# Kernel tuning notes

Hardware: AMD Instinct MI355X
Metric: run time of the kernel (lower is better)

Reference implementation:

```python
import jax, jax.numpy as jnp
import numpy as np

N_NODES = 50000
N_EDGES = 300000
IN_DIM = 2000
DF = 128
H1, H2, OUT_DIM, K = 256, 128, 32, 4


def gcn_conv(x, W, b, src, dst, ew):
    """PyG GCNConv with edge weights: add self-loops (weight 1), symmetric norm."""
    N = x.shape[0]
    loop = jnp.arange(N)
    src2 = jnp.concatenate([src, loop])
    dst2 = jnp.concatenate([dst, loop])
    ew2 = jnp.concatenate([ew, jnp.ones((N,), ew.dtype)])
    deg = jax.ops.segment_sum(ew2, dst2, num_segments=N)
    dinv = jnp.where(deg > 0, jax.lax.rsqrt(deg), 0.0)
    norm = dinv[src2] * ew2 * dinv[dst2]            # [E+N]
    h = x @ W                                       # [N, out]
    out = jax.ops.segment_sum(norm[:, None] * h[src2], dst2, num_segments=N)
    return out + b


def setup_inputs() -> dict:
    key = jax.random.key(0)
    ks = jax.random.split(key, 13)
    p = lambda k, shape, s=0.05: (jax.random.normal(k, shape, jnp.float32) * s)
    return {
        "X": jax.random.normal(ks[0], (N_NODES, IN_DIM), jnp.float32),
        "edge_index": jax.random.randint(ks[1], (2, N_EDGES), 0, N_NODES),
        "Wh": p(ks[2], (IN_DIM, DF)),
        "mlp_W1": p(ks[3], (K, 2 * DF, 2)),
        "mlp_b1": jnp.zeros((K, 2), jnp.float32),
        "mlp_W2": p(ks[4], (K, 2, 1)),
        "mlp_b2": jnp.zeros((K, 1), jnp.float32),
        "g1_W": p(ks[5], (DF, H1)),
        "g1_b": jnp.zeros((H1,), jnp.float32),
        "g2_W": p(ks[6], (H1, H2)),
        "g2_b": jnp.zeros((H2,), jnp.float32),
        "fc_W": p(ks[7], (H2, OUT_DIM)),
        "fc_b": jnp.zeros((OUT_DIM,), jnp.float32),
    }


def reference(X, edge_index, Wh, mlp_W1, mlp_b1, mlp_W2, mlp_b2,
              g1_W, g1_b, g2_W, g2_b, fc_W, fc_b):
    src, dst = edge_index[0], edge_index[1]
    h0 = X @ Wh                                          # [N, df]
    edge_h = jnp.concatenate([h0[src], h0[dst]], axis=1)  # [E, 2df]
    # all K per-edge MLPs at once: hidden dim is just 2
    hid = jax.nn.relu(jnp.einsum('ef,kfh->keh', edge_h, mlp_W1) + mlp_b1[:, None, :])
    Gk = jax.nn.sigmoid(jnp.einsum('keh,kho->keo', hid, mlp_W2) + mlp_b2[:, None, :])[..., 0]  # [K, E]

    def autoencoder(ew):
        z1 = jax.nn.relu(gcn_conv(h0, g1_W, g1_b, src, dst, ew))
        z2 = jax.nn.relu(gcn_conv(z1, g2_W, g2_b, src, dst, ew))
        return jnp.mean(z2, axis=0) @ fc_W + fc_b         # [out_dim]

    descriptors = jax.vmap(autoencoder)(Gk)               # [K, out_dim]
    return descriptors, Gk
```

## Files before the change

### kernel.cpp

```cpp
#include <hip/hip_runtime.h>

#define NN 50000
#define NE 300000
#define INDIM 2000
#define KPAD 2048

typedef float f32x4 __attribute__((ext_vector_type(4)));
typedef __bf16 bf16x8 __attribute__((ext_vector_type(8)));
typedef unsigned short u16x8 __attribute__((ext_vector_type(8)));

__device__ __forceinline__ unsigned short f2bf(float f) {
  union { float f; unsigned u; } v; v.f = f;
  unsigned r = v.u + 0x7FFFu + ((v.u >> 16) & 1u);
  return (unsigned short)(r >> 16);
}
__device__ __forceinline__ float bf2f(unsigned short h) {
  union { unsigned u; float f; } v; v.u = ((unsigned)h) << 16;
  return v.f;
}

__global__ __launch_bounds__(256) void prep_kernel(
    const float* __restrict__ Wh, const float* __restrict__ g1,
    const float* __restrict__ g2, const float* __restrict__ W1,
    unsigned short* __restrict__ WhT, unsigned short* __restrict__ g1T,
    unsigned short* __restrict__ g2T, float* __restrict__ Wc)
{
  int i = blockIdx.x * 256 + threadIdx.x;
  if (i < 128 * KPAD) {
    int n = i >> 11, k = i & (KPAD - 1);
    WhT[i] = (k < INDIM) ? f2bf(Wh[(size_t)k * 128 + n]) : (unsigned short)0;
    return;
  }
  i -= 128 * KPAD;
  if (i < 256 * 128) {
    int n = i >> 7, k = i & 127;
    g1T[i] = f2bf(g1[(size_t)k * 256 + n]);
    return;
  }
  i -= 256 * 128;
  if (i < 128 * 256) {
    int n = i >> 8, k = i & 255;
    g2T[i] = f2bf(g2[(size_t)k * 128 + n]);
    return;
  }
  i -= 128 * 256;
  if (i < 2048) {
    int f = i >> 4, o = i & 15;
    int k = (o & 7) >> 1, h = o & 1;
    int fr = (o < 8) ? f : (128 + f);
    Wc[i] = W1[(size_t)k * 512 + fr * 2 + h];
  }
}

template<int A_F32>
__global__ __launch_bounds__(256) void gemm_kernel(
    const void* __restrict__ Aptr, const unsigned short* __restrict__ BT,
    unsigned short* __restrict__ C, int M, int N, int Ka, int Kb, int nkb)
{
  __shared__ unsigned short Alds[128 * 64];
  __shared__ unsigned short Blds[128 * 64];
  const int tid = threadIdx.x, lane = tid & 63, wv = tid >> 6;
  const int mBase = blockIdx.x * 128, nBase = blockIdx.y * 128;
  const int wrow = (wv >> 1) * 64, wcol = (wv & 1) * 64;
  const int lr = lane >> 3, lk8 = (lane & 7) * 8;
  const int stIdx = (lr) * 64 + (((lane & 7) ^ lr) << 3);
  f32x4 acc[4][4] = {};

  for (int kb = 0; kb < nkb; ++kb) {
    int k0 = kb * 64;
    #pragma unroll
    for (int i = 0; i < 4; ++i) {
      int chunk = wv * 4 + i;
      int brow = chunk * 8 + lr;
      u16x8 v = *(const u16x8*)(BT + (size_t)(nBase + brow) * Kb + k0 + lk8);
      *(u16x8*)&Blds[chunk * 512 + stIdx] = v;
    }
    #pragma unroll
    for (int i = 0; i < 4; ++i) {
      int chunk = wv * 4 + i;
      int arow = chunk * 8 + lr;
      int rg = mBase + arow; if (rg > M - 1) rg = M - 1;
      u16x8 v;
      if (A_F32) {
        const float* Af = (const float*)Aptr;
        int kc = k0 + lk8; if (kc > Ka - 8) kc = Ka - 8;
        const float4* s = (const float4*)(Af + (size_t)rg * Ka + kc);
        float4 f0 = s[0], f1 = s[1];
        v[0]=f2bf(f0.x); v[1]=f2bf(f0.y); v[2]=f2bf(f0.z); v[3]=f2bf(f0.w);
        v[4]=f2bf(f1.x); v[5]=f2bf(f1.y); v[6]=f2bf(f1.z); v[7]=f2bf(f1.w);
      } else {
        const unsigned short* Ab = (const unsigned short*)Aptr;
        v = *(const u16x8*)(Ab + (size_t)rg * Ka + k0 + lk8);
      }
      *(u16x8*)&Alds[chunk * 512 + stIdx] = v;
    }
    __syncthreads();
    #pragma unroll
    for (int kk = 0; kk < 2; ++kk) {
      const int r16 = lane & 15;
      const int slot = kk * 4 + (lane >> 4);
      bf16x8 a[4], b[4];
      #pragma unroll
      for (int mf = 0; mf < 4; ++mf) {
        int row = wrow + mf * 16 + r16;
        a[mf] = __builtin_bit_cast(bf16x8,
            *(const u16x8*)&Alds[row * 64 + ((slot ^ (row & 7)) << 3)]);
      }
      #pragma unroll
      for (int nf = 0; nf < 4; ++nf) {
        int row = wcol + nf * 16 + r16;
        b[nf] = __builtin_bit_cast(bf16x8,
            *(const u16x8*)&Blds[row * 64 + ((slot ^ (row & 7)) << 3)]);
      }
      #pragma unroll
      for (int mf = 0; mf < 4; ++mf)
        #pragma unroll
        for (int nf = 0; nf < 4; ++nf)
          acc[mf][nf] = __builtin_amdgcn_mfma_f32_16x16x32_bf16(a[mf], b[nf], acc[mf][nf], 0, 0, 0);
    }
    __syncthreads();
  }

  const int r16 = lane & 15, r4 = (lane >> 4) * 4;
  #pragma unroll
  for (int mf = 0; mf < 4; ++mf) {
    #pragma unroll
    for (int j = 0; j < 4; ++j) {
      int row = mBase + wrow + mf * 16 + r4 + j;
      if (row < M) {
        #pragma unroll
        for (int nf = 0; nf < 4; ++nf) {
          int col = nBase + wcol + nf * 16 + r16;
          C[(size_t)row * N + col] = f2bf(acc[mf][nf][j]);
        }
      }
    }
  }
}

__global__ __launch_bounds__(256) void p_kernel(const unsigned short* __restrict__ h0,
    const float* __restrict__ Wc, float* __restrict__ P)
{
  __shared__ float wl[2048];
  for (int i = threadIdx.x; i < 2048; i += 256) wl[i] = Wc[i];
  __syncthreads();
  int n = blockIdx.x * 256 + threadIdx.x;
  if (n >= NN) return;
  const unsigned short* hr = h0 + (size_t)n * 128;
  float acc[16];
  #pragma unroll
  for (int o = 0; o < 16; ++o) acc[o] = 0.f;
  for (int f8 = 0; f8 < 128; f8 += 8) {
    u16x8 hv = *(const u16x8*)(hr + f8);
    #pragma unroll
    for (int j = 0; j < 8; ++j) {
      float v = bf2f(hv[j]);
      #pragma unroll
      for (int o = 0; o < 16; ++o) acc[o] += v * wl[(f8 + j) * 16 + o];
    }
  }
  #pragma unroll
  for (int o = 0; o < 16; ++o) P[(size_t)n * 16 + o] = acc[o];
}

__global__ __launch_bounds__(256) void init_kernel(float* deg, int* hist, float* colsum)
{
  int i = blockIdx.x * 256 + threadIdx.x;
  if (i < 4 * NN) deg[i] = 1.0f;
  if (i < NN) hist[i] = 0;
  if (i < 512) colsum[i] = 0.f;
}

__global__ __launch_bounds__(256) void gk_kernel(
    const int* __restrict__ ei, const float* __restrict__ P,
    const float* __restrict__ b1, const float* __restrict__ W2,
    const float* __restrict__ b2, float* __restrict__ GkOut,
    float4* __restrict__ Gk4, float* __restrict__ deg, int* __restrict__ hist)
{
  int e = blockIdx.x * 256 + threadIdx.x;
  if (e >= NE) return;
  int s = ei[e], d = ei[NE + e];
  const float4* Ps = (const float4*)(P + (size_t)s * 16);
  const float4* Pd = (const float4*)(P + (size_t)d * 16);
  float4 p1a = Ps[0], p1b = Ps[1];
  float4 p2a = Pd[2], p2b = Pd[3];
  float p1[8] = {p1a.x, p1a.y, p1a.z, p1a.w, p1b.x, p1b.y, p1b.z, p1b.w};
  float p2[8] = {p2a.x, p2a.y, p2a.z, p2a.w, p2b.x, p2b.y, p2b.z, p2b.w};
  float g[4];
  #pragma unroll
  for (int k = 0; k < 4; ++k) {
    float h0v = p1[2*k]   + p2[2*k]   + b1[2*k];
    float h1v = p1[2*k+1] + p2[2*k+1] + b1[2*k+1];
    h0v = h0v > 0.f ? h0v : 0.f;
    h1v = h1v > 0.f ? h1v : 0.f;
    float pre = h0v * W2[2*k] + h1v * W2[2*k+1] + b2[k];
    g[k] = 1.f / (1.f + expf(-pre));
    GkOut[(size_t)k * NE + e] = g[k];
    atomicAdd(&deg[k * NN + d], g[k]);
  }
  Gk4[e] = make_float4(g[0], g[1], g[2], g[3]);
  atomicAdd(&hist[d], 1);
}

__global__ __launch_bounds__(256) void scan1_kernel(const int* __restrict__ hist,
    int* __restrict__ excl, int* __restrict__ bsum)
{
  __shared__ int sm[256];
  int t = threadIdx.x, i = blockIdx.x * 256 + t;
  int v = (i < NN) ? hist[i] : 0;
  sm[t] = v;
  __syncthreads();
  for (int off = 1; off < 256; off <<= 1) {
    int y = (t >= off) ? sm[t - off] : 0;
    __syncthreads();
    sm[t] += y;
    __syncthreads();
  }
  if (i < NN) excl[i] = sm[t] - v;
  if (t == 255) bsum[blockIdx.x] = sm[255];
}

__global__ __launch_bounds__(256) void scan2_kernel(int* bsum, int nb)
{
  __shared__ int sm[256];
  int t = threadIdx.x;
  int v = (t < nb) ? bsum[t] : 0;
  sm[t] = v;
  __syncthreads();
  for (int off = 1; off < 256; off <<= 1) {
    int y = (t >= off) ? sm[t - off] : 0;
    __syncthreads();
    sm[t] += y;
    __syncthreads();
  }
  if (t < nb) bsum[t] = sm[t] - v;
}

__global__ __launch_bounds__(256) void scan3_kernel(int* __restrict__ rowstart,
    const int* __restrict__ bsum, int* __restrict__ cursor)
{
  int i = blockIdx.x * 256 + threadIdx.x;
  if (i < NN) {
    int v = rowstart[i] + bsum[blockIdx.x];
    rowstart[i] = v;
    cursor[i] = v;
  }
  if (i == 0) rowstart[NN] = NE;
}

__global__ __launch_bounds__(256) void dinv_kernel(const float* __restrict__ deg,
    float* __restrict__ dinv)
{
  int i = blockIdx.x * 256 + threadIdx.x;
  if (i < 4 * NN) dinv[i] = rsqrtf(deg[i]);
}

__global__ __launch_bounds__(256) void csr_kernel(const int* __restrict__ ei,
    int* __restrict__ cursor, int* __restrict__ csr_s, int* __restrict__ csr_e)
{
  int e = blockIdx.x * 256 + threadIdx.x;
  if (e >= NE) return;
  int s = ei[e], d = ei[NE + e];
  int pos = atomicAdd(&cursor[d], 1);
  csr_s[pos] = s;
  csr_e[pos] = e;
}

__global__ __launch_bounds__(256) void csrw_kernel(const int* __restrict__ csr_s,
    const int* __restrict__ csr_e, const float4* __restrict__ Gk4,
    const float* __restrict__ dinv, float4* __restrict__ w4)
{
  int p = blockIdx.x * 256 + threadIdx.x;
  if (p >= NE) return;
  int s = csr_s[p], e = csr_e[p];
  float4 g = Gk4[e];
  float4 w;
  w.x = g.x * dinv[0 * NN + s];
  w.y = g.y * dinv[1 * NN + s];
  w.z = g.z * dinv[2 * NN + s];
  w.w = g.w * dinv[3 * NN + s];
  w4[p] = w;
}

__global__ __launch_bounds__(256) void aggA_kernel(
    const unsigned short* __restrict__ H1, unsigned short* __restrict__ Z1,
    const float* __restrict__ dinv, const int* __restrict__ rowstart,
    const int* __restrict__ csr_s, const float4* __restrict__ w4,
    const float* __restrict__ g1b)
{
  const int lane = threadIdx.x & 63;
  const int wv = threadIdx.x >> 6;
  const int gw = blockIdx.x * 4 + wv;
  const int nw = gridDim.x * 4;
  const int c0 = lane * 4;
  float bb[4];
  #pragma unroll
  for (int c = 0; c < 4; ++c) bb[c] = g1b[c0 + c];
  for (int n = gw; n < NN; n += nw) {
    float dd[4];
    #pragma unroll
    for (int k = 0; k < 4; ++k) dd[k] = dinv[k * NN + n];
    uint2 sv = *(const uint2*)(H1 + (size_t)n * 256 + c0);
    float sf[4] = { bf2f((unsigned short)(sv.x & 0xFFFF)), bf2f((unsigned short)(sv.x >> 16)),
                    bf2f((unsigned short)(sv.y & 0xFFFF)), bf2f((unsigned short)(sv.y >> 16)) };
    float acc[4][4];
    #pragma unroll
    for (int k = 0; k < 4; ++k)
      #pragma unroll
      for (int c = 0; c < 4; ++c) acc[k][c] = dd[k] * sf[c];
    int rs = rowstart[n], re = rowstart[n + 1];
    for (int p = rs; p < re; ++p) {
      int s = csr_s[p];
      float4 w = w4[p];
      uint2 hv = *(const uint2*)(H1 + (size_t)s * 256 + c0);
      float hf[4] = { bf2f((unsigned short)(hv.x & 0xFFFF)), bf2f((unsigned short)(hv.x >> 16)),
                      bf2f((unsigned short)(hv.y & 0xFFFF)), bf2f((unsigned short)(hv.y >> 16)) };
      #pragma unroll
      for (int c = 0; c < 4; ++c) {
        acc[0][c] += w.x * hf[c];
        acc[1][c] += w.y * hf[c];
        acc[2][c] += w.z * hf[c];
        acc[3][c] += w.w * hf[c];
      }
    }
    #pragma unroll
    for (int k = 0; k < 4; ++k) {
      uint2 ov;
      float z0 = dd[k] * acc[k][0] + bb[0]; z0 = z0 > 0.f ? z0 : 0.f;
      float z1 = dd[k] * acc[k][1] + bb[1]; z1 = z1 > 0.f ? z1 : 0.f;
      float z2 = dd[k] * acc[k][2] + bb[2]; z2 = z2 > 0.f ? z2 : 0.f;
      float z3 = dd[k] * acc[k][3] + bb[3]; z3 = z3 > 0.f ? z3 : 0.f;
      ov.x = (unsigned)f2bf(z0) | ((unsigned)f2bf(z1) << 16);
      ov.y = (unsigned)f2bf(z2) | ((unsigned)f2bf(z3) << 16);
      *(uint2*)(Z1 + ((size_t)k * NN + n) * 256 + c0) = ov;
    }
  }
}

__global__ __launch_bounds__(256) void aggB_kernel(
    const unsigned short* __restrict__ Y2, const float* __restrict__ dinv,
    const int* __restrict__ rowstart, const int* __restrict__ csr_s,
    const float* __restrict__ w4s, const float* __restrict__ g2b,
    float* __restrict__ colsum)
{
  const int k = blockIdx.y;
  const int lane = threadIdx.x & 63;
  const int wv = threadIdx.x >> 6;
  const int gw = blockIdx.x * 4 + wv;
  const int nw = gridDim.x * 4;
  const int c0 = lane * 2;
  const float bb0 = g2b[c0], bb1 = g2b[c0 + 1];
  const unsigned short* Yk = Y2 + (size_t)k * NN * 128;
  const float* dk = dinv + (size_t)k * NN;
  float s0 = 0.f, s1 = 0.f;
  for (int n = gw; n < NN; n += nw) {
    float dd = dk[n];
    unsigned selfv = *(const unsigned*)(Yk + (size_t)n * 128 + c0);
    float a0 = dd * bf2f((unsigned short)(selfv & 0xFFFFu));
    float a1 = dd * bf2f((unsigned short)(selfv >> 16));
    int rs = rowstart[n], re = rowstart[n + 1];
    for (int p = rs; p < re; ++p) {
      int s = csr_s[p];
      float w = w4s[(size_t)p * 4 + k];
      unsigned hv = *(const unsigned*)(Yk + (size_t)s * 128 + c0);
      a0 += w * bf2f((unsigned short)(hv & 0xFFFFu));
      a1 += w * bf2f((unsigned short)(hv >> 16));
    }
    a0 = dd * a0 + bb0;
    a1 = dd * a1 + bb1;
    s0 += a0 > 0.f ? a0 : 0.f;
    s1 += a1 > 0.f ? a1 : 0.f;
  }
  __shared__ float lsum[128];
  if (threadIdx.x < 128) lsum[threadIdx.x] = 0.f;
  __syncthreads();
  atomicAdd(&lsum[c0], s0);
  atomicAdd(&lsum[c0 + 1], s1);
  __syncthreads();
  if (threadIdx.x < 128) atomicAdd(&colsum[k * 128 + threadIdx.x], lsum[threadIdx.x]);
}

__global__ void desc_kernel(const float* __restrict__ colsum,
    const float* __restrict__ fcW, const float* __restrict__ fcb,
    float* __restrict__ out)
{
  int t = threadIdx.x;
  if (t >= 128) return;
  int k = t >> 5, o = t & 31;
  float acc = 0.f;
  for (int c = 0; c < 128; ++c)
    acc += colsum[k * 128 + c] * fcW[c * 32 + o];
  out[t] = acc * (1.f / (float)NN) + fcb[o];
}

extern "C" void kernel_launch(void* const* d_in, const int* in_sizes, int n_in,
                              void* d_out, int out_size, void* d_ws, size_t ws_size,
                              hipStream_t stream)
{
  (void)in_sizes; (void)n_in; (void)out_size; (void)ws_size;
  const float* X   = (const float*)d_in[0];
  const int*   ei  = (const int*)d_in[1];
  const float* Wh  = (const float*)d_in[2];
  const float* W1  = (const float*)d_in[3];
  const float* b1  = (const float*)d_in[4];
  const float* W2  = (const float*)d_in[5];
  const float* b2  = (const float*)d_in[6];
  const float* g1W = (const float*)d_in[7];
  const float* g1b = (const float*)d_in[8];
  const float* g2W = (const float*)d_in[9];
  const float* g2b = (const float*)d_in[10];
  const float* fcW = (const float*)d_in[11];
  const float* fcb = (const float*)d_in[12];
  float* out = (float*)d_out;

  char* ws = (char*)d_ws;
  size_t off = 0;
  auto alloc = [&](size_t bytes) -> void* {
    void* p = ws + off; off += (bytes + 255) & ~(size_t)255; return p;
  };
  unsigned short* WhT = (unsigned short*)alloc((size_t)128 * KPAD * 2);
  unsigned short* g1T = (unsigned short*)alloc((size_t)256 * 128 * 2);
  unsigned short* g2T = (unsigned short*)alloc((size_t)128 * 256 * 2);
  float* Wc  = (float*)alloc(2048 * 4);
  unsigned short* h0 = (unsigned short*)alloc((size_t)NN * 128 * 2);
  unsigned short* H1 = (unsigned short*)alloc((size_t)NN * 256 * 2);
  float* P   = (float*)alloc((size_t)NN * 16 * 4);
  float* deg = (float*)alloc((size_t)4 * NN * 4);
  float* dinv= (float*)alloc((size_t)4 * NN * 4);
  int* hist  = (int*)alloc((size_t)NN * 4);
  int* rowst = (int*)alloc((size_t)(NN + 1) * 4);
  int* cursor= (int*)alloc((size_t)NN * 4);
  int* bsum  = (int*)alloc(256 * 4);
  int* csr_s = (int*)alloc((size_t)NE * 4);
  int* csr_e = (int*)alloc((size_t)NE * 4);
  float4* Gk4 = (float4*)alloc((size_t)NE * 16);
  float4* w4  = (float4*)alloc((size_t)NE * 16);
  unsigned short* Z1 = (unsigned short*)alloc((size_t)4 * NN * 256 * 2);
  unsigned short* Y2 = (unsigned short*)alloc((size_t)4 * NN * 128 * 2);
  float* colsum = (float*)alloc(512 * 4);

  float* GkOut = out + 128;
  const int gEdge = (NE + 255) / 256;

  prep_kernel<<<(128*KPAD + 256*128 + 128*256 + 2048 + 255)/256, 256, 0, stream>>>(
      Wh, g1W, g2W, W1, WhT, g1T, g2T, Wc);
  init_kernel<<<(4*NN + 255)/256, 256, 0, stream>>>(deg, hist, colsum);
  gemm_kernel<1><<<dim3(391, 1), 256, 0, stream>>>(
      X, WhT, h0, NN, 128, INDIM, KPAD, KPAD / 64);
  gemm_kernel<0><<<dim3(391, 2), 256, 0, stream>>>(
      h0, g1T, H1, NN, 256, 128, 128, 2);
  p_kernel<<<196, 256, 0, stream>>>(h0, Wc, P);
  gk_kernel<<<gEdge, 256, 0, stream>>>(ei, P, b1, W2, b2, GkOut, Gk4, deg, hist);
  scan1_kernel<<<196, 256, 0, stream>>>(hist, rowst, bsum);
  scan2_kernel<<<1, 256, 0, stream>>>(bsum, 196);
  scan3_kernel<<<196, 256, 0, stream>>>(rowst, bsum, cursor);
  dinv_kernel<<<(4*NN + 255)/256, 256, 0, stream>>>(deg, dinv);
  csr_kernel<<<gEdge, 256, 0, stream>>>(ei, cursor, csr_s, csr_e);
  csrw_kernel<<<gEdge, 256, 0, stream>>>(csr_s, csr_e, Gk4, dinv, w4);
  aggA_kernel<<<2048, 256, 0, stream>>>(H1, Z1, dinv, rowst, csr_s, w4, g1b);
  gemm_kernel<0><<<dim3(1563, 1), 256, 0, stream>>>(
      Z1, g2T, Y2, 4 * NN, 128, 256, 256, 4);
  aggB_kernel<<<dim3(1024, 4), 256, 0, stream>>>(
      Y2, dinv, rowst, csr_s, (const float*)w4, g2b, colsum);
  desc_kernel<<<1, 128, 0, stream>>>(colsum, fcW, fcb, out);
}
```

Measured before the change: 943.4 us.

## Interleave per-K buffers node-major, fuse aggB across K, use global_load_lds in GEMM

```diff
diff --git a/kernel.cpp b/kernel.cpp
--- a/kernel.cpp
+++ b/kernel.cpp
@@ -8,11 +8,12 @@
 typedef float f32x4 __attribute__((ext_vector_type(4)));
 typedef __bf16 bf16x8 __attribute__((ext_vector_type(8)));
 typedef unsigned short u16x8 __attribute__((ext_vector_type(8)));
+typedef unsigned int u32;
+typedef __attribute__((address_space(3))) u32 lds_u32;
+typedef const __attribute__((address_space(1))) u32 glb_u32;
 
 __device__ __forceinline__ unsigned short f2bf(float f) {
-  union { float f; unsigned u; } v; v.f = f;
-  unsigned r = v.u + 0x7FFFu + ((v.u >> 16) & 1u);
-  return (unsigned short)(r >> 16);
+  return __builtin_bit_cast(unsigned short, (__bf16)f);
 }
 __device__ __forceinline__ float bf2f(unsigned short h) {
   union { unsigned u; float f; } v; v.u = ((unsigned)h) << 16;
@@ -63,7 +64,8 @@
   const int mBase = blockIdx.x * 128, nBase = blockIdx.y * 128;
   const int wrow = (wv >> 1) * 64, wcol = (wv & 1) * 64;
   const int lr = lane >> 3, lk8 = (lane & 7) * 8;
-  const int stIdx = (lr) * 64 + (((lane & 7) ^ lr) << 3);
+  const int swzCol = (((lane & 7) ^ lr) << 3);
+  const int stIdx = lr * 64 + swzCol;
   f32x4 acc[4][4] = {};
 
   for (int kb = 0; kb < nkb; ++kb) {
@@ -71,28 +73,35 @@
     #pragma unroll
     for (int i = 0; i < 4; ++i) {
       int chunk = wv * 4 + i;
-      int brow = chunk * 8 + lr;
-      u16x8 v = *(const u16x8*)(BT + (size_t)(nBase + brow) * Kb + k0 + lk8);
-      *(u16x8*)&Blds[chunk * 512 + stIdx] = v;
-    }
-    #pragma unroll
-    for (int i = 0; i < 4; ++i) {
-      int chunk = wv * 4 + i;
-      int arow = chunk * 8 + lr;
-      int rg = mBase + arow; if (rg > M - 1) rg = M - 1;
-      u16x8 v;
-      if (A_F32) {
-        const float* Af = (const float*)Aptr;
+      int brow = nBase + chunk * 8 + lr;
+      __builtin_amdgcn_global_load_lds(
+          (glb_u32*)(BT + (size_t)brow * Kb + k0 + swzCol),
+          (lds_u32*)&Blds[chunk * 512 + lane * 8], 16, 0, 0);
+    }
+    if (A_F32) {
+      const float* Af = (const float*)Aptr;
+      #pragma unroll
+      for (int i = 0; i < 4; ++i) {
+        int chunk = wv * 4 + i;
+        int rg = mBase + chunk * 8 + lr; if (rg > M - 1) rg = M - 1;
         int kc = k0 + lk8; if (kc > Ka - 8) kc = Ka - 8;
         const float4* s = (const float4*)(Af + (size_t)rg * Ka + kc);
         float4 f0 = s[0], f1 = s[1];
+        u16x8 v;
         v[0]=f2bf(f0.x); v[1]=f2bf(f0.y); v[2]=f2bf(f0.z); v[3]=f2bf(f0.w);
         v[4]=f2bf(f1.x); v[5]=f2bf(f1.y); v[6]=f2bf(f1.z); v[7]=f2bf(f1.w);
-      } else {
-        const unsigned short* Ab = (const unsigned short*)Aptr;
-        v = *(const u16x8*)(Ab + (size_t)rg * Ka + k0 + lk8);
-      }
-      *(u16x8*)&Alds[chunk * 512 + stIdx] = v;
+        *(u16x8*)&Alds[chunk * 512 + stIdx] = v;
+      }
+    } else {
+      const unsigned short* Ab = (const unsigned short*)Aptr;
+      #pragma unroll
+      for (int i = 0; i < 4; ++i) {
+        int chunk = wv * 4 + i;
+        int rg = mBase + chunk * 8 + lr; if (rg > M - 1) rg = M - 1;
+        __builtin_amdgcn_global_load_lds(
+            (glb_u32*)(Ab + (size_t)rg * Ka + k0 + swzCol),
+            (lds_u32*)&Alds[chunk * 512 + lane * 8], 16, 0, 0);
+      }
     }
     __syncthreads();
     #pragma unroll
@@ -196,7 +205,7 @@
     float pre = h0v * W2[2*k] + h1v * W2[2*k+1] + b2[k];
     g[k] = 1.f / (1.f + expf(-pre));
     GkOut[(size_t)k * NE + e] = g[k];
-    atomicAdd(&deg[k * NN + d], g[k]);
+    atomicAdd(&deg[(size_t)d * 4 + k], g[k]);
   }
   Gk4[e] = make_float4(g[0], g[1], g[2], g[3]);
   atomicAdd(&hist[d], 1);
@@ -268,23 +277,24 @@
 
 __global__ __launch_bounds__(256) void csrw_kernel(const int* __restrict__ csr_s,
     const int* __restrict__ csr_e, const float4* __restrict__ Gk4,
-    const float* __restrict__ dinv, float4* __restrict__ w4)
+    const float4* __restrict__ dinv4, float4* __restrict__ w4)
 {
   int p = blockIdx.x * 256 + threadIdx.x;
   if (p >= NE) return;
   int s = csr_s[p], e = csr_e[p];
   float4 g = Gk4[e];
+  float4 dv = dinv4[s];
   float4 w;
-  w.x = g.x * dinv[0 * NN + s];
-  w.y = g.y * dinv[1 * NN + s];
-  w.z = g.z * dinv[2 * NN + s];
-  w.w = g.w * dinv[3 * NN + s];
+  w.x = g.x * dv.x;
+  w.y = g.y * dv.y;
+  w.z = g.z * dv.z;
+  w.w = g.w * dv.w;
   w4[p] = w;
 }
 
 __global__ __launch_bounds__(256) void aggA_kernel(
     const unsigned short* __restrict__ H1, unsigned short* __restrict__ Z1,
-    const float* __restrict__ dinv, const int* __restrict__ rowstart,
+    const float4* __restrict__ dinv4, const int* __restrict__ rowstart,
     const int* __restrict__ csr_s, const float4* __restrict__ w4,
     const float* __restrict__ g1b)
 {
@@ -297,9 +307,8 @@
   #pragma unroll
   for (int c = 0; c < 4; ++c) bb[c] = g1b[c0 + c];
   for (int n = gw; n < NN; n += nw) {
-    float dd[4];
-    #pragma unroll
-    for (int k = 0; k < 4; ++k) dd[k] = dinv[k * NN + n];
+    float4 dv = dinv4[n];
+    float dd[4] = { dv.x, dv.y, dv.z, dv.w };
     uint2 sv = *(const uint2*)(H1 + (size_t)n * 256 + c0);
     float sf[4] = { bf2f((unsigned short)(sv.x & 0xFFFF)), bf2f((unsigned short)(sv.x >> 16)),
                     bf2f((unsigned short)(sv.y & 0xFFFF)), bf2f((unsigned short)(sv.y >> 16)) };
@@ -332,52 +341,55 @@
       float z3 = dd[k] * acc[k][3] + bb[3]; z3 = z3 > 0.f ? z3 : 0.f;
       ov.x = (unsigned)f2bf(z0) | ((unsigned)f2bf(z1) << 16);
       ov.y = (unsigned)f2bf(z2) | ((unsigned)f2bf(z3) << 16);
-      *(uint2*)(Z1 + ((size_t)k * NN + n) * 256 + c0) = ov;
+      *(uint2*)(Z1 + ((size_t)n * 4 + k) * 256 + c0) = ov;
     }
   }
 }
 
 __global__ __launch_bounds__(256) void aggB_kernel(
-    const unsigned short* __restrict__ Y2, const float* __restrict__ dinv,
+    const unsigned short* __restrict__ Y2, const float4* __restrict__ dinv4,
     const int* __restrict__ rowstart, const int* __restrict__ csr_s,
-    const float* __restrict__ w4s, const float* __restrict__ g2b,
+    const float4* __restrict__ w4, const float* __restrict__ g2b,
     float* __restrict__ colsum)
 {
-  const int k = blockIdx.y;
   const int lane = threadIdx.x & 63;
   const int wv = threadIdx.x >> 6;
   const int gw = blockIdx.x * 4 + wv;
   const int nw = gridDim.x * 4;
-  const int c0 = lane * 2;
-  const float bb0 = g2b[c0], bb1 = g2b[c0 + 1];
-  const unsigned short* Yk = Y2 + (size_t)k * NN * 128;
-  const float* dk = dinv + (size_t)k * NN;
-  float s0 = 0.f, s1 = 0.f;
+  const int kk = lane >> 4;
+  const int c0 = (lane & 15) * 8;
+  float bb[8];
+  #pragma unroll
+  for (int j = 0; j < 8; ++j) bb[j] = g2b[c0 + j];
+  float s[8] = {};
   for (int n = gw; n < NN; n += nw) {
-    float dd = dk[n];
-    unsigned selfv = *(const unsigned*)(Yk + (size_t)n * 128 + c0);
-    float a0 = dd * bf2f((unsigned short)(selfv & 0xFFFFu));
-    float a1 = dd * bf2f((unsigned short)(selfv >> 16));
+    float4 dv = dinv4[n];
+    float dd = kk == 0 ? dv.x : kk == 1 ? dv.y : kk == 2 ? dv.z : dv.w;
+    u16x8 sv = *(const u16x8*)(Y2 + (size_t)n * 512 + lane * 8);
+    float a[8];
+    #pragma unroll
+    for (int j = 0; j < 8; ++j) a[j] = dd * bf2f(sv[j]);
     int rs = rowstart[n], re = rowstart[n + 1];
     for (int p = rs; p < re; ++p) {
-      int s = csr_s[p];
-      float w = w4s[(size_t)p * 4 + k];
-      unsigned hv = *(const unsigned*)(Yk + (size_t)s * 128 + c0);
-      a0 += w * bf2f((unsigned short)(hv & 0xFFFFu));
-      a1 += w * bf2f((unsigned short)(hv >> 16));
-    }
-    a0 = dd * a0 + bb0;
-    a1 = dd * a1 + bb1;
-    s0 += a0 > 0.f ? a0 : 0.f;
-    s1 += a1 > 0.f ? a1 : 0.f;
-  }
-  __shared__ float lsum[128];
-  if (threadIdx.x < 128) lsum[threadIdx.x] = 0.f;
+      int src = csr_s[p];
+      float4 w4v = w4[p];
+      float w = kk == 0 ? w4v.x : kk == 1 ? w4v.y : kk == 2 ? w4v.z : w4v.w;
+      u16x8 hv = *(const u16x8*)(Y2 + (size_t)src * 512 + lane * 8);
+      #pragma unroll
+      for (int j = 0; j < 8; ++j) a[j] += w * bf2f(hv[j]);
+    }
+    #pragma unroll
+    for (int j = 0; j < 8; ++j) {
+      float z = dd * a[j] + bb[j];
+      s[j] += z > 0.f ? z : 0.f;
+    }
+  }
+  __shared__ float lsum[4 * 512];
+  #pragma unroll
+  for (int j = 0; j < 8; ++j) lsum[wv * 512 + kk * 128 + c0 + j] = s[j];
   __syncthreads();
-  atomicAdd(&lsum[c0], s0);
-  atomicAdd(&lsum[c0 + 1], s1);
-  __syncthreads();
-  if (threadIdx.x < 128) atomicAdd(&colsum[k * 128 + threadIdx.x], lsum[threadIdx.x]);
+  for (int i = threadIdx.x; i < 512; i += 256)
+    atomicAdd(&colsum[i], lsum[i] + lsum[512 + i] + lsum[1024 + i] + lsum[1536 + i]);
 }
 
 __global__ void desc_kernel(const float* __restrict__ colsum,
@@ -456,11 +468,11 @@
   scan3_kernel<<<196, 256, 0, stream>>>(rowst, bsum, cursor);
   dinv_kernel<<<(4*NN + 255)/256, 256, 0, stream>>>(deg, dinv);
   csr_kernel<<<gEdge, 256, 0, stream>>>(ei, cursor, csr_s, csr_e);
-  csrw_kernel<<<gEdge, 256, 0, stream>>>(csr_s, csr_e, Gk4, dinv, w4);
-  aggA_kernel<<<2048, 256, 0, stream>>>(H1, Z1, dinv, rowst, csr_s, w4, g1b);
+  csrw_kernel<<<gEdge, 256, 0, stream>>>(csr_s, csr_e, Gk4, (const float4*)dinv, w4);
+  aggA_kernel<<<2048, 256, 0, stream>>>(H1, Z1, (const float4*)dinv, rowst, csr_s, w4, g1b);
   gemm_kernel<0><<<dim3(1563, 1), 256, 0, stream>>>(
       Z1, g2T, Y2, 4 * NN, 128, 256, 256, 4);
-  aggB_kernel<<<dim3(1024, 4), 256, 0, stream>>>(
-      Y2, dinv, rowst, csr_s, (const float*)w4, g2b, colsum);
+  aggB_kernel<<<2048, 256, 0, stream>>>(
+      Y2, (const float4*)dinv, rowst, csr_s, w4, g2b, colsum);
   desc_kernel<<<1, 128, 0, stream>>>(colsum, fcW, fcb, out);
 }
```

After: 891.5 us. -5.5%, faster.
